# Performance work log

Measured on AMD Instinct MI355X. Metric: run time of the kernel, lower is better.

## Reference

```python
import jax, jax.numpy as jnp
import numpy as np

N_NODES = 50000


def _gcn_conv(x, W, b, src, dst, n):
    """PyG GCNConv: add self-loops, symmetric normalization, sum-aggregate."""
    h = x @ W  # [N, out_dim] dense transform first (out_dim <= in_dim path)
    loop = jnp.arange(n, dtype=src.dtype)
    src_sl = jnp.concatenate([src, loop])
    dst_sl = jnp.concatenate([dst, loop])
    # degree computed on destination nodes (incl. self-loops)
    deg = jax.ops.segment_sum(jnp.ones_like(dst_sl, dtype=h.dtype), dst_sl, num_segments=n)
    dinv = jnp.where(deg > 0, jax.lax.rsqrt(deg), 0.0)
    norm = dinv[src_sl] * dinv[dst_sl]  # [E+N]
    msgs = h[src_sl] * norm[:, None]  # gather + scale, [E+N, out_dim]
    out = jax.ops.segment_sum(msgs, dst_sl, num_segments=n)  # scatter-add
    return out + b


def setup_inputs() -> dict:
    key = jax.random.key(0)
    k0, k1, k2, k3 = jax.random.split(key, 4)
    d = 256
    E = 400000
    scale = 1.0 / np.sqrt(d)
    x = jax.random.normal(k0, (N_NODES, d), dtype=jnp.float32)
    edge_index = jax.random.randint(k1, (2, E), 0, N_NODES, dtype=jnp.int64)
    W1 = jax.random.normal(k2, (d, d), dtype=jnp.float32) * scale
    b1 = jnp.zeros((d,), dtype=jnp.float32)
    W2 = jax.random.normal(k3, (d, d), dtype=jnp.float32) * scale
    b2 = jnp.zeros((d,), dtype=jnp.float32)
    return {"x": x, "edge_index": edge_index, "W1": W1, "b1": b1, "W2": W2, "b2": b2}


def reference(x, edge_index, W1, b1, W2, b2):
    src, dst = edge_index[0], edge_index[1]
    h = _gcn_conv(x, W1, b1, src, dst, N_NODES)
    h = jax.nn.relu(h)
    h = _gcn_conv(h, W2, b2, src, dst, N_NODES)
    h = jax.nn.relu(h)
    return h
```

## Files before the change

### kernel.cpp

```cpp
#include <hip/hip_runtime.h>
#include <stdint.h>

typedef __bf16 bf16_t;
typedef bf16_t bf16x4 __attribute__((ext_vector_type(4)));
typedef bf16_t bf16x8 __attribute__((ext_vector_type(8)));
typedef float f32x4 __attribute__((ext_vector_type(4)));

#define DIM 256
#define NNODES 50000
#define NPANEL 8
#define PDIM 32

__device__ __forceinline__ int detect_f64(const int* __restrict__ ei) {
    int v = ei[2 * (threadIdx.x & 63) + 1];
    unsigned long long m = __ballot(v == 0);
    return __popcll(m) > 32;
}

__device__ __forceinline__ int load_edge(const int* __restrict__ ei, int E, int f64,
                                         int which , int e) {
    int v = f64 ? ei[(size_t)which * 2 * E + 2 * (size_t)e]
                : ei[(size_t)which * E + (size_t)e];
    return min(max(v, 0), NNODES - 1);
}


__global__ void hist_kernel(const int* __restrict__ ei, int E, int* __restrict__ counts) {
    int f64 = detect_f64(ei);
    int e = blockIdx.x * blockDim.x + threadIdx.x;
    if (e < E) atomicAdd(&counts[load_edge(ei, E, f64, 1, e)], 1);
}

__global__ __launch_bounds__(256) void scanA_kernel(const int* __restrict__ counts,
                                                    int* __restrict__ offsets,
                                                    int* __restrict__ bsums, int n) {
    __shared__ int sm[256];
    int b = blockIdx.x, t = threadIdx.x;
    int idx = b * 256 + t;
    int v = (idx < n) ? counts[idx] : 0;
    sm[t] = v;
    __syncthreads();
    #pragma unroll
    for (int off = 1; off < 256; off <<= 1) {
        int u = (t >= off) ? sm[t - off] : 0;
        __syncthreads();
        sm[t] += u;
        __syncthreads();
    }
    if (idx < n) offsets[idx + 1] = sm[t];
    if (t == 255) bsums[b] = sm[255];
}

__global__ __launch_bounds__(256) void scanB_kernel(int* __restrict__ bsums, int nb) {
    __shared__ int sm[256];
    int t = threadIdx.x;
    int v = (t < nb) ? bsums[t] : 0;
    sm[t] = v;
    __syncthreads();
    #pragma unroll
    for (int off = 1; off < 256; off <<= 1) {
        int u = (t >= off) ? sm[t - off] : 0;
        __syncthreads();
        sm[t] += u;
        __syncthreads();
    }
    if (t < nb) bsums[t] = sm[t] - v;
}

__global__ __launch_bounds__(256) void scanC_kernel(const int* __restrict__ counts,
                                                    const int* __restrict__ bsums,
                                                    int* __restrict__ offsets,
                                                    float* __restrict__ dinv,
                                                    int* __restrict__ cursor, int n) {
    int b = blockIdx.x;
    int idx = b * 256 + threadIdx.x;
    if (idx == 0) offsets[0] = 0;
    if (idx < n) {
        int incl = offsets[idx + 1] + bsums[b];
        offsets[idx + 1] = incl;
        cursor[idx] = incl - counts[idx];
        dinv[idx] = rsqrtf((float)(counts[idx] + 1));
    }
}

__global__ void scatter_kernel(const int* __restrict__ ei, int E,
                               const float* __restrict__ dinv, int* __restrict__ cursor,
                               int2* __restrict__ csr_e) {
    int f64 = detect_f64(ei);
    int e = blockIdx.x * blockDim.x + threadIdx.x;
    if (e < E) {
        int s = load_edge(ei, E, f64, 0, e);
        int d = load_edge(ei, E, f64, 1, e);
        int pos = atomicAdd(&cursor[d], 1);
        if (pos >= 0 && pos < E) {
            int2 v;
            v.x = s;
            v.y = __float_as_int(dinv[s] * dinv[d]);
            csr_e[pos] = v;
        }
    }
}


__global__ void convert_w_kernel(const float* __restrict__ W1, const float* __restrict__ W2,
                                 bf16_t* __restrict__ Wf1, bf16_t* __restrict__ Wf2) {
    const float* W = blockIdx.y ? W2 : W1;
    bf16_t* Wf = blockIdx.y ? Wf2 : Wf1;
    int k = blockIdx.x, n = threadIdx.x;
    int s = k >> 5, quad = (k >> 3) & 3, j = k & 7;
    int nt = n >> 4, m = n & 15;
    Wf[s * 8192 + (nt * 64 + quad * 16 + m) * 8 + j] = (bf16_t)W[k * DIM + n];
}


template <bool F32A>
__global__ __launch_bounds__(256, 4) void gemm_kernel(const void* __restrict__ Xv,
                                                      const bf16_t* __restrict__ Wf,
                                                      bf16_t* __restrict__ Hp, int tiles) {
    __shared__ bf16_t sB[8192];
    int tid = threadIdx.x;
    int wave = tid >> 6, lane = tid & 63;
    int m = lane & 15, quad = lane >> 4;
    int tile = blockIdx.x * 4 + wave;
    bool active = tile < tiles;
    int arow = (min(tile, tiles - 1)) * 16 + m;

    f32x4 acc[16] = {};

    for (int s = 0; s < 8; s++) {
        __syncthreads();
        {
            const bf16x8* g = (const bf16x8*)Wf + s * 1024;
            bf16x8* d = (bf16x8*)sB;
            #pragma unroll
            for (int it = 0; it < 4; it++) d[tid + it * 256] = g[tid + it * 256];
        }
        __syncthreads();

        bf16x8 a;
        if (F32A) {
            const f32x4* xp = (const f32x4*)((const float*)Xv + (size_t)arow * DIM + s * 32 + quad * 8);
            f32x4 x0 = xp[0], x1 = xp[1];
            #pragma unroll
            for (int j = 0; j < 4; j++) { a[j] = (bf16_t)x0[j]; a[j + 4] = (bf16_t)x1[j]; }
        } else {
            a = *(const bf16x8*)((const bf16_t*)Xv + ((size_t)s * NNODES + arow) * PDIM + quad * 8);
        }

        #pragma unroll
        for (int nt = 0; nt < 16; nt++) {
            bf16x8 b = *(const bf16x8*)(sB + nt * 512 + lane * 8);
            acc[nt] = __builtin_amdgcn_mfma_f32_16x16x32_bf16(a, b, acc[nt], 0, 0, 0);
        }
    }

    if (active) {
        int rowb = tile * 16 + quad * 4;
        #pragma unroll
        for (int nt = 0; nt < 16; nt++) {
            size_t pbase = ((size_t)(nt >> 1) * NNODES) * PDIM + (nt & 1) * 16 + m;
            #pragma unroll
            for (int r = 0; r < 4; r++) {
                Hp[pbase + (size_t)(rowb + r) * PDIM] = (bf16_t)acc[nt][r];
            }
        }
    }
}


template <int OUT_BF16P>
__global__ __launch_bounds__(256) void aggregate_kernel(const bf16_t* __restrict__ Hp,
                                                        const int* __restrict__ offsets,
                                                        const int2* __restrict__ csr_e,
                                                        const float* __restrict__ dinv,
                                                        const float* __restrict__ bias,
                                                        void* __restrict__ outv, int n) {
    int p = blockIdx.x & 7;
    int chunk = blockIdx.x >> 3;
    int wave = threadIdx.x >> 6, lane = threadIdx.x & 63;
    int g = lane >> 3, c = lane & 7;
    int i = chunk * 32 + wave * 8 + g;
    if (i >= n) return;

    auto cvt = [](bf16x4 v) -> f32x4 {
        f32x4 r;
        #pragma unroll
        for (int j = 0; j < 4; j++) r[j] = (float)v[j];
        return r;
    };

    const bf16_t* Hpan = Hp + (size_t)p * ((size_t)NNODES * PDIM);
    float dii = dinv[i];
    f32x4 acc = cvt(*(const bf16x4*)(Hpan + (size_t)i * PDIM + c * 4)) * (dii * dii);
    int e0 = offsets[i], e1 = offsets[i + 1];

    for (int e = e0; e < e1; e += 8) {
        int2 ed;
        if (e + c < e1) {
            ed = csr_e[e + c];
        } else {
            ed.x = i;
            ed.y = 0;
        }
        int s[8]; float w[8];
        #pragma unroll
        for (int j = 0; j < 8; j++) {
            int srcLane = (lane & 56) + j;
            s[j] = __shfl(ed.x, srcLane, 64);
            w[j] = __uint_as_float((unsigned)__shfl(ed.y, srcLane, 64));
        }
        bf16x4 h[8];
        #pragma unroll
        for (int j = 0; j < 8; j++) {
            h[j] = *(const bf16x4*)(Hpan + (size_t)s[j] * PDIM + c * 4);
        }
        #pragma unroll
        for (int j = 0; j < 8; j++) acc += cvt(h[j]) * w[j];
    }

    acc += *(const f32x4*)(bias + p * PDIM + c * 4);
    #pragma unroll
    for (int j = 0; j < 4; j++) acc[j] = fmaxf(acc[j], 0.0f);

    if (OUT_BF16P) {
        bf16x4 o;
        #pragma unroll
        for (int j = 0; j < 4; j++) o[j] = (bf16_t)acc[j];
        *(bf16x4*)((bf16_t*)outv + (size_t)p * NNODES * PDIM + (size_t)i * PDIM + c * 4) = o;
    } else {
        *(f32x4*)((float*)outv + (size_t)i * DIM + p * PDIM + c * 4) = acc;
    }
}


extern "C" void kernel_launch(void* const* d_in, const int* in_sizes, int n_in,
                              void* d_out, int out_size, void* d_ws, size_t ws_size,
                              hipStream_t stream) {
    const float* x  = (const float*)d_in[0];
    const int*   ei = (const int*)d_in[1];
    const float* W1 = (const float*)d_in[2];
    const float* b1 = (const float*)d_in[3];
    const float* W2 = (const float*)d_in[4];
    const float* b2 = (const float*)d_in[5];
    float* out = (float*)d_out;

    const int n = NNODES;
    const int E = in_sizes[1] / 2;
    const int nb = (n + 255) / 256;

    char* ws = (char*)d_ws;
    size_t off = 0;
    auto alloc = [&](size_t bytes) -> char* {
        char* p = ws + off;
        off += (bytes + 255) & ~(size_t)255;
        return p;
    };
    float*  dinv     = (float*)alloc((size_t)n * 4);
    int*    counts   = (int*)alloc((size_t)n * 4);
    int*    offsets  = (int*)alloc((size_t)(n + 1) * 4);
    int*    cursor   = (int*)alloc((size_t)n * 4);
    int*    bsums    = (int*)alloc((size_t)nb * 4);
    int2*   csr_e    = (int2*)alloc((size_t)E * 8);
    bf16_t* Wf1      = (bf16_t*)alloc((size_t)DIM * DIM * 2);
    bf16_t* Wf2      = (bf16_t*)alloc((size_t)DIM * DIM * 2);
    bf16_t* P        = (bf16_t*)alloc((size_t)n * DIM * 2);
    bf16_t* X2       = (bf16_t*)alloc((size_t)n * DIM * 2);

    hipMemsetAsync(counts, 0, (size_t)n * 4, stream);
    hist_kernel<<<(E + 255) / 256, 256, 0, stream>>>(ei, E, counts);
    scanA_kernel<<<nb, 256, 0, stream>>>(counts, offsets, bsums, n);
    scanB_kernel<<<1, 256, 0, stream>>>(bsums, nb);
    scanC_kernel<<<nb, 256, 0, stream>>>(counts, bsums, offsets, dinv, cursor, n);
    scatter_kernel<<<(E + 255) / 256, 256, 0, stream>>>(ei, E, dinv, cursor, csr_e);

    convert_w_kernel<<<dim3(DIM, 2), DIM, 0, stream>>>(W1, W2, Wf1, Wf2);

    int tiles = (n + 15) / 16;
    int gemm_blocks = (tiles + 3) / 4;
    int agg_blocks = NPANEL * ((n + 31) / 32);

    gemm_kernel<true><<<gemm_blocks, 256, 0, stream>>>(x, Wf1, P, tiles);
    aggregate_kernel<1><<<agg_blocks, 256, 0, stream>>>(P, offsets, csr_e, dinv, b1, X2, n);
    gemm_kernel<false><<<gemm_blocks, 256, 0, stream>>>(X2, Wf2, P, tiles);
    aggregate_kernel<0><<<agg_blocks, 256, 0, stream>>>(P, offsets, csr_e, dinv, b2, out, n);
}
```

Before: 259.0 us.

## Replace paneled feature layout with row-major and one row per half-wave aggregation

Drops the 8-panel bf16 layout and stores intermediate features row-major, with the GEMM writing and reading full 512-byte rows. The aggregation now gives each node to 32 lanes, each loading 16 bytes per neighbor, so one gather covers the whole row in a single coalesced access. Edge indices and weights are read as uniform loads per edge, which removes the cross-lane shuffles. In exchange the panel-level L2 locality is lost, since each pass now touches the full feature matrix, and the GEMM's scattered 2-byte output stores stay in place.

```diff
diff --git a/kernel.cpp b/kernel.cpp
--- a/kernel.cpp
+++ b/kernel.cpp
@@ -8,8 +8,6 @@
 
 #define DIM 256
 #define NNODES 50000
-#define NPANEL 8
-#define PDIM 32
 
 __device__ __forceinline__ int detect_f64(const int* __restrict__ ei) {
     int v = ei[2 * (threadIdx.x & 63) + 1];
@@ -116,7 +114,7 @@
 template <bool F32A>
 __global__ __launch_bounds__(256, 4) void gemm_kernel(const void* __restrict__ Xv,
                                                       const bf16_t* __restrict__ Wf,
-                                                      bf16_t* __restrict__ Hp, int tiles) {
+                                                      bf16_t* __restrict__ H, int tiles) {
     __shared__ bf16_t sB[8192];
     int tid = threadIdx.x;
     int wave = tid >> 6, lane = tid & 63;
@@ -144,7 +142,7 @@
             #pragma unroll
             for (int j = 0; j < 4; j++) { a[j] = (bf16_t)x0[j]; a[j + 4] = (bf16_t)x1[j]; }
         } else {
-            a = *(const bf16x8*)((const bf16_t*)Xv + ((size_t)s * NNODES + arow) * PDIM + quad * 8);
+            a = *(const bf16x8*)((const bf16_t*)Xv + (size_t)arow * DIM + s * 32 + quad * 8);
         }
 
         #pragma unroll
@@ -158,29 +156,29 @@
         int rowb = tile * 16 + quad * 4;
         #pragma unroll
         for (int nt = 0; nt < 16; nt++) {
-            size_t pbase = ((size_t)(nt >> 1) * NNODES) * PDIM + (nt & 1) * 16 + m;
             #pragma unroll
             for (int r = 0; r < 4; r++) {
-                Hp[pbase + (size_t)(rowb + r) * PDIM] = (bf16_t)acc[nt][r];
+                H[(size_t)(rowb + r) * DIM + nt * 16 + m] = (bf16_t)acc[nt][r];
             }
         }
     }
 }
 
 
-template <int OUT_BF16P>
-__global__ __launch_bounds__(256) void aggregate_kernel(const bf16_t* __restrict__ Hp,
+template <int OUT_BF16>
+__global__ __launch_bounds__(256) void aggregate_kernel(const bf16_t* __restrict__ H,
                                                         const int* __restrict__ offsets,
                                                         const int2* __restrict__ csr_e,
                                                         const float* __restrict__ dinv,
                                                         const float* __restrict__ bias,
                                                         void* __restrict__ outv, int n) {
-    int p = blockIdx.x & 7;
-    int chunk = blockIdx.x >> 3;
-    int wave = threadIdx.x >> 6, lane = threadIdx.x & 63;
-    int g = lane >> 3, c = lane & 7;
-    int i = chunk * 32 + wave * 8 + g;
+    int wg = threadIdx.x >> 5;
+    int l = threadIdx.x & 31;
+    int i = blockIdx.x * 8 + wg;
     if (i >= n) return;
+
+    const char* Hb = (const char*)H;
+    int doff = l * 16;
 
     auto cvt = [](bf16x4 v) -> f32x4 {
         f32x4 r;
@@ -188,47 +186,75 @@
         for (int j = 0; j < 4; j++) r[j] = (float)v[j];
         return r;
     };
-
-    const bf16_t* Hpan = Hp + (size_t)p * ((size_t)NNODES * PDIM);
+    auto lo4 = [](bf16x8 v) -> bf16x4 { return __builtin_shufflevector(v, v, 0, 1, 2, 3); };
+    auto hi4 = [](bf16x8 v) -> bf16x4 { return __builtin_shufflevector(v, v, 4, 5, 6, 7); };
+
     float dii = dinv[i];
-    f32x4 acc = cvt(*(const bf16x4*)(Hpan + (size_t)i * PDIM + c * 4)) * (dii * dii);
+    bf16x8 selfv = *(const bf16x8*)(Hb + ((size_t)i << 9) + doff);
+    f32x4 acc0 = cvt(lo4(selfv)) * (dii * dii);
+    f32x4 acc1 = cvt(hi4(selfv)) * (dii * dii);
+
     int e0 = offsets[i], e1 = offsets[i + 1];
-
-    for (int e = e0; e < e1; e += 8) {
-        int2 ed;
-        if (e + c < e1) {
-            ed = csr_e[e + c];
-        } else {
-            ed.x = i;
-            ed.y = 0;
-        }
-        int s[8]; float w[8];
-        #pragma unroll
-        for (int j = 0; j < 8; j++) {
-            int srcLane = (lane & 56) + j;
-            s[j] = __shfl(ed.x, srcLane, 64);
-            w[j] = __uint_as_float((unsigned)__shfl(ed.y, srcLane, 64));
-        }
-        bf16x4 h[8];
-        #pragma unroll
-        for (int j = 0; j < 8; j++) {
-            h[j] = *(const bf16x4*)(Hpan + (size_t)s[j] * PDIM + c * 4);
-        }
-        #pragma unroll
-        for (int j = 0; j < 8; j++) acc += cvt(h[j]) * w[j];
-    }
-
-    acc += *(const f32x4*)(bias + p * PDIM + c * 4);
+    int e = e0;
+    for (; e + 8 <= e1; e += 8) {
+        unsigned s[8]; float w[8];
+        #pragma unroll
+        for (int j = 0; j < 8; j++) {
+            int2 t = csr_e[e + j];
+            s[j] = min((unsigned)t.x, (unsigned)(NNODES - 1));
+            w[j] = __int_as_float(t.y);
+        }
+        bf16x8 h[8];
+        #pragma unroll
+        for (int j = 0; j < 8; j++) {
+            h[j] = *(const bf16x8*)(Hb + ((size_t)s[j] << 9) + doff);
+        }
+        #pragma unroll
+        for (int j = 0; j < 8; j++) {
+            acc0 += cvt(lo4(h[j])) * w[j];
+            acc1 += cvt(hi4(h[j])) * w[j];
+        }
+    }
+    if (e < e1) {
+        unsigned s[8]; float w[8];
+        #pragma unroll
+        for (int j = 0; j < 8; j++) {
+            bool valid = (e + j) < e1;
+            int2 t = csr_e[valid ? e + j : e];
+            if (!valid) { t.x = i; t.y = 0; }
+            s[j] = min((unsigned)t.x, (unsigned)(NNODES - 1));
+            w[j] = __int_as_float(t.y);
+        }
+        bf16x8 h[8];
+        #pragma unroll
+        for (int j = 0; j < 8; j++) {
+            h[j] = *(const bf16x8*)(Hb + ((size_t)s[j] << 9) + doff);
+        }
+        #pragma unroll
+        for (int j = 0; j < 8; j++) {
+            acc0 += cvt(lo4(h[j])) * w[j];
+            acc1 += cvt(hi4(h[j])) * w[j];
+        }
+    }
+
+    const f32x4* bp = (const f32x4*)(bias + l * 8);
+    acc0 += bp[0];
+    acc1 += bp[1];
     #pragma unroll
-    for (int j = 0; j < 4; j++) acc[j] = fmaxf(acc[j], 0.0f);
-
-    if (OUT_BF16P) {
-        bf16x4 o;
-        #pragma unroll
-        for (int j = 0; j < 4; j++) o[j] = (bf16_t)acc[j];
-        *(bf16x4*)((bf16_t*)outv + (size_t)p * NNODES * PDIM + (size_t)i * PDIM + c * 4) = o;
+    for (int j = 0; j < 4; j++) {
+        acc0[j] = fmaxf(acc0[j], 0.0f);
+        acc1[j] = fmaxf(acc1[j], 0.0f);
+    }
+
+    if (OUT_BF16) {
+        bf16x8 o;
+        #pragma unroll
+        for (int j = 0; j < 4; j++) { o[j] = (bf16_t)acc0[j]; o[j + 4] = (bf16_t)acc1[j]; }
+        *(bf16x8*)((bf16_t*)outv + (size_t)i * DIM + l * 8) = o;
     } else {
-        *(f32x4*)((float*)outv + (size_t)i * DIM + p * PDIM + c * 4) = acc;
+        float* op = (float*)outv + (size_t)i * DIM + l * 8;
+        *(f32x4*)op = acc0;
+        *(f32x4*)(op + 4) = acc1;
     }
 }
 
@@ -277,7 +303,7 @@
 
     int tiles = (n + 15) / 16;
     int gemm_blocks = (tiles + 3) / 4;
-    int agg_blocks = NPANEL * ((n + 31) / 32);
+    int agg_blocks = (n + 7) / 8;
 
     gemm_kernel<true><<<gemm_blocks, 256, 0, stream>>>(x, Wf1, P, tiles);
     aggregate_kernel<1><<<agg_blocks, 256, 0, stream>>>(P, offsets, csr_e, dinv, b1, X2, n);
```

Measured after the change: 260.6 us. No clear change (+0.6%).

## Make aggregation persistent with XCD-affine per-panel work queues

Applied to the files above, without the earlier changes.

Replaces the static grid over (panel, node-chunk) with a persistent grid of 2048 blocks. Each block reads its XCD id from a hardware register and pulls node chunks from an atomic queue for the feature panel tied to that XCD, moving to other panels once its own is drained. The aim is to keep each 32-column panel's gather traffic inside one XCD's L2 so the random source-row reads hit cache more often. The cost is an atomic and two block barriers per chunk, plus a dependence on hardware XCD numbering. The queue counters are zeroed by widening the existing memset.

```diff
diff --git a/kernel.cpp b/kernel.cpp
--- a/kernel.cpp
+++ b/kernel.cpp
@@ -174,13 +174,13 @@
                                                         const int2* __restrict__ csr_e,
                                                         const float* __restrict__ dinv,
                                                         const float* __restrict__ bias,
-                                                        void* __restrict__ outv, int n) {
-    int p = blockIdx.x & 7;
-    int chunk = blockIdx.x >> 3;
-    int wave = threadIdx.x >> 6, lane = threadIdx.x & 63;
-    int g = lane >> 3, c = lane & 7;
-    int i = chunk * 32 + wave * 8 + g;
-    if (i >= n) return;
+                                                        void* __restrict__ outv,
+                                                        int* __restrict__ qctr, int n) {
+    __shared__ int s_t;
+    const int CPP = (NNODES + 31) / 32;
+    int xcd;
+    asm volatile("s_getreg_b32 %0, hwreg(20, 0, 32)" : "=s"(xcd));
+    xcd &= 7;
 
     auto cvt = [](bf16x4 v) -> f32x4 {
         f32x4 r;
@@ -189,46 +189,62 @@
         return r;
     };
 
-    const bf16_t* Hpan = Hp + (size_t)p * ((size_t)NNODES * PDIM);
-    float dii = dinv[i];
-    f32x4 acc = cvt(*(const bf16x4*)(Hpan + (size_t)i * PDIM + c * 4)) * (dii * dii);
-    int e0 = offsets[i], e1 = offsets[i + 1];
-
-    for (int e = e0; e < e1; e += 8) {
-        int2 ed;
-        if (e + c < e1) {
-            ed = csr_e[e + c];
-        } else {
-            ed.x = i;
-            ed.y = 0;
-        }
-        int s[8]; float w[8];
-        #pragma unroll
-        for (int j = 0; j < 8; j++) {
-            int srcLane = (lane & 56) + j;
-            s[j] = __shfl(ed.x, srcLane, 64);
-            w[j] = __uint_as_float((unsigned)__shfl(ed.y, srcLane, 64));
-        }
-        bf16x4 h[8];
-        #pragma unroll
-        for (int j = 0; j < 8; j++) {
-            h[j] = *(const bf16x4*)(Hpan + (size_t)s[j] * PDIM + c * 4);
-        }
-        #pragma unroll
-        for (int j = 0; j < 8; j++) acc += cvt(h[j]) * w[j];
-    }
-
-    acc += *(const f32x4*)(bias + p * PDIM + c * 4);
-    #pragma unroll
-    for (int j = 0; j < 4; j++) acc[j] = fmaxf(acc[j], 0.0f);
-
-    if (OUT_BF16P) {
-        bf16x4 o;
-        #pragma unroll
-        for (int j = 0; j < 4; j++) o[j] = (bf16_t)acc[j];
-        *(bf16x4*)((bf16_t*)outv + (size_t)p * NNODES * PDIM + (size_t)i * PDIM + c * 4) = o;
-    } else {
-        *(f32x4*)((float*)outv + (size_t)i * DIM + p * PDIM + c * 4) = acc;
+    int probe = 0;
+    while (probe < 8) {
+        int q = (xcd + probe) & 7;
+        if (threadIdx.x == 0) s_t = atomicAdd(&qctr[q], 1);
+        __syncthreads();
+        int t = s_t;
+        __syncthreads();
+        if (t >= CPP) { probe++; continue; }
+
+        int p = q;
+        int wave = threadIdx.x >> 6, lane = threadIdx.x & 63;
+        int g = lane >> 3, c = lane & 7;
+        int i = t * 32 + wave * 8 + g;
+        if (i < n) {
+            const bf16_t* Hpan = Hp + (size_t)p * ((size_t)NNODES * PDIM);
+            float dii = dinv[i];
+            f32x4 acc = cvt(*(const bf16x4*)(Hpan + (size_t)i * PDIM + c * 4)) * (dii * dii);
+            int e0 = offsets[i], e1 = offsets[i + 1];
+
+            for (int e = e0; e < e1; e += 8) {
+                int2 ed;
+                if (e + c < e1) {
+                    ed = csr_e[e + c];
+                } else {
+                    ed.x = i;
+                    ed.y = 0;
+                }
+                int s[8]; float w[8];
+                #pragma unroll
+                for (int j = 0; j < 8; j++) {
+                    int srcLane = (lane & 56) + j;
+                    s[j] = __shfl(ed.x, srcLane, 64);
+                    w[j] = __uint_as_float((unsigned)__shfl(ed.y, srcLane, 64));
+                }
+                bf16x4 h[8];
+                #pragma unroll
+                for (int j = 0; j < 8; j++) {
+                    h[j] = *(const bf16x4*)(Hpan + (size_t)s[j] * PDIM + c * 4);
+                }
+                #pragma unroll
+                for (int j = 0; j < 8; j++) acc += cvt(h[j]) * w[j];
+            }
+
+            acc += *(const f32x4*)(bias + p * PDIM + c * 4);
+            #pragma unroll
+            for (int j = 0; j < 4; j++) acc[j] = fmaxf(acc[j], 0.0f);
+
+            if (OUT_BF16P) {
+                bf16x4 o;
+                #pragma unroll
+                for (int j = 0; j < 4; j++) o[j] = (bf16_t)acc[j];
+                *(bf16x4*)((bf16_t*)outv + (size_t)p * NNODES * PDIM + (size_t)i * PDIM + c * 4) = o;
+            } else {
+                *(f32x4*)((float*)outv + (size_t)i * DIM + p * PDIM + c * 4) = acc;
+            }
+        }
     }
 }
 
@@ -257,6 +273,7 @@
     };
     float*  dinv     = (float*)alloc((size_t)n * 4);
     int*    counts   = (int*)alloc((size_t)n * 4);
+    int*    qctr     = (int*)alloc(256);
     int*    offsets  = (int*)alloc((size_t)(n + 1) * 4);
     int*    cursor   = (int*)alloc((size_t)n * 4);
     int*    bsums    = (int*)alloc((size_t)nb * 4);
@@ -266,7 +283,9 @@
     bf16_t* P        = (bf16_t*)alloc((size_t)n * DIM * 2);
     bf16_t* X2       = (bf16_t*)alloc((size_t)n * DIM * 2);
 
-    hipMemsetAsync(counts, 0, (size_t)n * 4, stream);
+    size_t cb = (((size_t)n * 4) + 255) & ~(size_t)255;
+    hipMemsetAsync(counts, 0, cb + 256, stream);
+
     hist_kernel<<<(E + 255) / 256, 256, 0, stream>>>(ei, E, counts);
     scanA_kernel<<<nb, 256, 0, stream>>>(counts, offsets, bsums, n);
     scanB_kernel<<<1, 256, 0, stream>>>(bsums, nb);
@@ -277,10 +296,12 @@
 
     int tiles = (n + 15) / 16;
     int gemm_blocks = (tiles + 3) / 4;
-    int agg_blocks = NPANEL * ((n + 31) / 32);
+    int agg_blocks = 2048;
 
     gemm_kernel<true><<<gemm_blocks, 256, 0, stream>>>(x, Wf1, P, tiles);
-    aggregate_kernel<1><<<agg_blocks, 256, 0, stream>>>(P, offsets, csr_e, dinv, b1, X2, n);
+    aggregate_kernel<1><<<agg_blocks, 256, 0, stream>>>(P, offsets, csr_e, dinv, b1, X2,
+                                                        qctr, n);
     gemm_kernel<false><<<gemm_blocks, 256, 0, stream>>>(X2, Wf2, P, tiles);
-    aggregate_kernel<0><<<agg_blocks, 256, 0, stream>>>(P, offsets, csr_e, dinv, b2, out, n);
-}
+    aggregate_kernel<0><<<agg_blocks, 256, 0, stream>>>(P, offsets, csr_e, dinv, b2, out,
+                                                        qctr + 8, n);
+}
```

After: 851.0 us. 3.29x slower.
